# Kernel tuning notes

Hardware: AMD Instinct MI355X
Metric: run time of the kernel (lower is better)

## Reference

```python
import jax, jax.numpy as jnp
import numpy as np

N_NODES = 10000
N_EDGES = 640000
EMB_DIM = 128
NUM_LAYERS = 4
EPS_GIN = 0.0   # Tokenizer init eps
BN_EPS = 1e-5


def setup_inputs() -> dict:
    key = jax.random.key(0)
    k1, k2, k3 = jax.random.split(key, 3)
    x = jax.random.normal(k1, (N_NODES, EMB_DIM), dtype=jnp.float32)
    src = jax.random.randint(k2, (N_EDGES,), 0, N_NODES)
    dst = jax.random.randint(k3, (N_EDGES,), 0, N_NODES)
    gamma = jnp.ones((NUM_LAYERS, EMB_DIM), dtype=jnp.float32)
    beta = jnp.zeros((NUM_LAYERS, EMB_DIM), dtype=jnp.float32)
    return {"x": x, "gamma": gamma, "beta": beta, "src": src, "dst": dst}


def reference(x, gamma, beta, src, dst):
    # Tokenizer forward: num_layer x (NonParaGINConv -> BatchNorm1d), JK='last'
    n = x.shape[0]
    h = x
    for l in range(NUM_LAYERS):
        # GIN: neigh = sum over in-edges of source features (copy_u + fn.sum)
        neigh = jax.ops.segment_sum(h[src], dst, num_segments=n)
        h = (1.0 + EPS_GIN) * h + neigh
        # BatchNorm1d, training mode: biased batch statistics over nodes
        mu = jnp.mean(h, axis=0)
        var = jnp.var(h, axis=0)
        h = (h - mu) * jax.lax.rsqrt(var + BN_EPS) * gamma[l] + beta[l]
    return h  # JK == 'last'
```

## Files before the change

kernel.cpp:

```cpp
#include <hip/hip_runtime.h>

#define DIM 128
#define BN_EPS_F 1e-5f
#define NSLICE 16
#define MAXN 10240
#define CHUNKS 256

typedef unsigned int u32;
typedef unsigned short u16;

__device__ __forceinline__ float bflo(u32 w) {
    union { u32 u; float f; } c; c.u = w << 16; return c.f;
}
__device__ __forceinline__ float bfhi(u32 w) {
    union { u32 u; float f; } c; c.u = w & 0xffff0000u; return c.f;
}
__device__ __forceinline__ u32 packbf(float x, float y) {
    union { float f; u32 u; } ax, ay; ax.f = x; ay.f = y;
    u32 xr = (ax.u + 0x7fffu + ((ax.u >> 16) & 1u)) >> 16;
    u32 yr = (ay.u + 0x7fffu + ((ay.u >> 16) & 1u)) >> 16;
    return xr | (yr << 16);
}


__global__ __launch_bounds__(256) void chunkhist_kernel(const int* __restrict__ dst,
                                                        int* __restrict__ hist,
                                                        int n, int E, int chunk) {
    __shared__ int bins[MAXN];
    int tid = threadIdx.x;
    for (int i = tid; i < n; i += 256) bins[i] = 0;
    __syncthreads();
    int e0 = blockIdx.x * chunk;
    int e1 = min(e0 + chunk, E);
    for (int e = e0 + tid; e < e1; e += 256) atomicAdd(&bins[dst[e]], 1);
    __syncthreads();
    int* out = hist + (size_t)blockIdx.x * n;
    for (int i = tid; i < n; i += 256) out[i] = bins[i];
}

__global__ __launch_bounds__(256) void chunkscan_kernel(const int* __restrict__ hist,
                                                        int* __restrict__ chunkpref,
                                                        int* __restrict__ counts, int n) {
    int bin = blockIdx.x * 256 + threadIdx.x;
    if (bin >= n) return;
    const int* hp = hist + bin;
    int* cp = chunkpref + bin;
    int run = 0;
#pragma unroll 32
    for (int b = 0; b < CHUNKS; b++) {
        int v = hp[(size_t)b * n];
        cp[(size_t)b * n] = run;
        run += v;
    }
    counts[bin] = run;
}

__global__ __launch_bounds__(1024) void scan_kernel(const int* __restrict__ counts,
                                                    int* __restrict__ prowptr, int n) {
    __shared__ int sums[1024];
    const int CH = 16;
    int t = threadIdx.x;
    int base = t * CH;
    int local[CH];
    int s = 0;
#pragma unroll
    for (int i = 0; i < CH; i++) {
        int idx = base + i;
        local[i] = s;
        if (idx < n) s += (counts[idx] + 15) & ~15;
    }
    sums[t] = s;
    __syncthreads();
    for (int off = 1; off < 1024; off <<= 1) {
        int v = (t >= off) ? sums[t - off] : 0;
        __syncthreads();
        sums[t] += v;
        __syncthreads();
    }
    int prev = (t > 0) ? sums[t - 1] : 0;
#pragma unroll
    for (int i = 0; i < CH; i++) {
        int idx = base + i;
        if (idx < n) prowptr[idx] = prev + local[i];
    }
    if (t == 1023) prowptr[n] = sums[1023];
}

__global__ __launch_bounds__(256) void misc_kernel(const float* __restrict__ x,
                                                   u16* __restrict__ xb,
                                                   u16* __restrict__ r0,
                                                   u16* __restrict__ r1,
                                                   const int* __restrict__ prowptr,
                                                   const int* __restrict__ counts,
                                                   int* __restrict__ srcsorted,
                                                   float* __restrict__ gstats,
                                                   int total4, int n,
                                                   int nb_cvt, int nb_pad, int gtotal) {
    int bid = blockIdx.x;
    int tid = threadIdx.x;
    if (bid < nb_cvt) {
        int i = bid * 256 + tid;
        if (i < total4) {
            float4 v = ((const float4*)x)[i];
            uint2 w;
            w.x = packbf(v.x, v.y);
            w.y = packbf(v.z, v.w);
            *(uint2*)(xb + (size_t)i * 4) = w;
        } else {
            int j = i - total4;
            if (j < 96) {
                u16* t = (j < 32) ? xb : ((j < 64) ? r0 : r1);
                uint2 z; z.x = 0; z.y = 0;
                *(uint2*)(t + (size_t)n * DIM + (j & 31) * 4) = z;
            }
        }
    } else if (bid < nb_cvt + nb_pad) {
        int i = (bid - nb_cvt) * 256 + tid;
        if (i < n) {
            int pstart = prowptr[i];
            int c = counts[i];
            int p = (c + 15) & ~15;
            for (int k = c; k < p; k++) srcsorted[pstart + k] = n;
        }
    } else {
        int i = (bid - nb_cvt - nb_pad) * 256 + tid;
        if (i < gtotal) gstats[i] = 0.f;
    }
}

__global__ __launch_bounds__(256) void scatter_kernel(const int* __restrict__ src,
                                                      const int* __restrict__ dst,
                                                      const int* __restrict__ prowptr,
                                                      const int* __restrict__ chunkpref,
                                                      int* __restrict__ srcsorted,
                                                      int n, int E, int chunk) {
    __shared__ int cur[MAXN];
    int tid = threadIdx.x;
    const int* cp = chunkpref + (size_t)blockIdx.x * n;
    for (int i = tid; i < n; i += 256) cur[i] = prowptr[i] + cp[i];
    __syncthreads();
    int e0 = blockIdx.x * chunk;
    int e1 = min(e0 + chunk, E);
    for (int e = e0 + tid; e < e1; e += 256) {
        int d = dst[e];
        int pos = atomicAdd(&cur[d], 1);
        srcsorted[pos] = src[e];
    }
}

template <int USE_AB>
__global__ __launch_bounds__(256) void gather_kernel(
    const u16* __restrict__ hin, u16* __restrict__ hout,
    const int* __restrict__ prowptr, const int* __restrict__ counts,
    const int* __restrict__ srcs,
    const float* __restrict__ stats_in, float* __restrict__ stats_out,
    const float* __restrict__ gamma, const float* __restrict__ beta,
    int n, float inv_n) {
    __shared__ float ab_s[2 * DIM];
    __shared__ float part[2][DIM];
    __shared__ float ls[4][DIM];
    __shared__ float lq[4][DIM];
    int tid = threadIdx.x;
    int wid = tid >> 6;
    int node = blockIdx.x * 4 + wid;
    int lane = tid & 63;
    int grp = lane >> 4;
    int sub = lane & 15;

    if (USE_AB) {
        int c = tid & 127;
        int which = tid >> 7;
        const float* basep = stats_in + which * NSLICE * DIM + c;
        float acc = 0.f;
#pragma unroll
        for (int k = 0; k < NSLICE; k++) acc += basep[k * DIM];
        part[which][c] = acc;
        __syncthreads();
        if (tid < DIM) {
            float mu = part[0][tid] * inv_n;
            float var = part[1][tid] * inv_n - mu * mu;
            float av = gamma[tid] * rsqrtf(var + BN_EPS_F);
            ab_s[tid] = av;
            ab_s[DIM + tid] = beta[tid] - mu * av;
        }
        __syncthreads();
    }

    float r[8];
#pragma unroll
    for (int k = 0; k < 8; k++) r[k] = 0.f;

    if (node < n) {
        int start = prowptr[node];
        int pend = prowptr[node + 1];
        int deg = counts[node];
        const u16* hsub = hin + sub * 8;
        float acc[8];
#pragma unroll
        for (int k = 0; k < 8; k++) acc[k] = 0.f;

        int eb = start;
        for (; eb + 32 <= pend; eb += 32) {
            int e0 = eb + grp * 4;
            int s0 = srcs[e0 + 0];
            int s1 = srcs[e0 + 1];
            int s2 = srcs[e0 + 2];
            int s3 = srcs[e0 + 3];
            int s4 = srcs[e0 + 16];
            int s5 = srcs[e0 + 17];
            int s6 = srcs[e0 + 18];
            int s7 = srcs[e0 + 19];
            uint4 v0 = *(const uint4*)(hsub + (size_t)s0 * DIM);
            uint4 v1 = *(const uint4*)(hsub + (size_t)s1 * DIM);
            uint4 v2 = *(const uint4*)(hsub + (size_t)s2 * DIM);
            uint4 v3 = *(const uint4*)(hsub + (size_t)s3 * DIM);
            uint4 v4 = *(const uint4*)(hsub + (size_t)s4 * DIM);
            uint4 v5 = *(const uint4*)(hsub + (size_t)s5 * DIM);
            uint4 v6 = *(const uint4*)(hsub + (size_t)s6 * DIM);
            uint4 v7 = *(const uint4*)(hsub + (size_t)s7 * DIM);
            acc[0] += ((bflo(v0.x) + bflo(v1.x)) + (bflo(v2.x) + bflo(v3.x))) +
                      ((bflo(v4.x) + bflo(v5.x)) + (bflo(v6.x) + bflo(v7.x)));
            acc[1] += ((bfhi(v0.x) + bfhi(v1.x)) + (bfhi(v2.x) + bfhi(v3.x))) +
                      ((bfhi(v4.x) + bfhi(v5.x)) + (bfhi(v6.x) + bfhi(v7.x)));
            acc[2] += ((bflo(v0.y) + bflo(v1.y)) + (bflo(v2.y) + bflo(v3.y))) +
                      ((bflo(v4.y) + bflo(v5.y)) + (bflo(v6.y) + bflo(v7.y)));
            acc[3] += ((bfhi(v0.y) + bfhi(v1.y)) + (bfhi(v2.y) + bfhi(v3.y))) +
                      ((bfhi(v4.y) + bfhi(v5.y)) + (bfhi(v6.y) + bfhi(v7.y)));
            acc[4] += ((bflo(v0.z) + bflo(v1.z)) + (bflo(v2.z) + bflo(v3.z))) +
                      ((bflo(v4.z) + bflo(v5.z)) + (bflo(v6.z) + bflo(v7.z)));
            acc[5] += ((bfhi(v0.z) + bfhi(v1.z)) + (bfhi(v2.z) + bfhi(v3.z))) +
                      ((bfhi(v4.z) + bfhi(v5.z)) + (bfhi(v6.z) + bfhi(v7.z)));
            acc[6] += ((bflo(v0.w) + bflo(v1.w)) + (bflo(v2.w) + bflo(v3.w))) +
                      ((bflo(v4.w) + bflo(v5.w)) + (bflo(v6.w) + bflo(v7.w)));
            acc[7] += ((bfhi(v0.w) + bfhi(v1.w)) + (bfhi(v2.w) + bfhi(v3.w))) +
                      ((bfhi(v4.w) + bfhi(v5.w)) + (bfhi(v6.w) + bfhi(v7.w)));
        }
        if (eb < pend) {
            int e0 = eb + grp * 4;
            int s0 = srcs[e0 + 0];
            int s1 = srcs[e0 + 1];
            int s2 = srcs[e0 + 2];
            int s3 = srcs[e0 + 3];
            uint4 v0 = *(const uint4*)(hsub + (size_t)s0 * DIM);
            uint4 v1 = *(const uint4*)(hsub + (size_t)s1 * DIM);
            uint4 v2 = *(const uint4*)(hsub + (size_t)s2 * DIM);
            uint4 v3 = *(const uint4*)(hsub + (size_t)s3 * DIM);
            acc[0] += (bflo(v0.x) + bflo(v1.x)) + (bflo(v2.x) + bflo(v3.x));
            acc[1] += (bfhi(v0.x) + bfhi(v1.x)) + (bfhi(v2.x) + bfhi(v3.x));
            acc[2] += (bflo(v0.y) + bflo(v1.y)) + (bflo(v2.y) + bflo(v3.y));
            acc[3] += (bfhi(v0.y) + bfhi(v1.y)) + (bfhi(v2.y) + bfhi(v3.y));
            acc[4] += (bflo(v0.z) + bflo(v1.z)) + (bflo(v2.z) + bflo(v3.z));
            acc[5] += (bfhi(v0.z) + bfhi(v1.z)) + (bfhi(v2.z) + bfhi(v3.z));
            acc[6] += (bflo(v0.w) + bflo(v1.w)) + (bflo(v2.w) + bflo(v3.w));
            acc[7] += (bfhi(v0.w) + bfhi(v1.w)) + (bfhi(v2.w) + bfhi(v3.w));
        }
#pragma unroll
        for (int k = 0; k < 8; k++) {
            acc[k] += __shfl_xor(acc[k], 16);
            acc[k] += __shfl_xor(acc[k], 32);
        }

        uint4 sv = *(const uint4*)(hin + (size_t)node * DIM + sub * 8);
        float self[8] = {bflo(sv.x), bfhi(sv.x), bflo(sv.y), bfhi(sv.y),
                         bflo(sv.z), bfhi(sv.z), bflo(sv.w), bfhi(sv.w)};
        float degp1 = 1.0f + (float)deg;

        float av[8], bv[8];
        if (USE_AB) {
            float4 a0 = *(const float4*)(ab_s + sub * 8);
            float4 a1 = *(const float4*)(ab_s + sub * 8 + 4);
            float4 b0 = *(const float4*)(ab_s + DIM + sub * 8);
            float4 b1 = *(const float4*)(ab_s + DIM + sub * 8 + 4);
            av[0] = a0.x; av[1] = a0.y; av[2] = a0.z; av[3] = a0.w;
            av[4] = a1.x; av[5] = a1.y; av[6] = a1.z; av[7] = a1.w;
            bv[0] = b0.x; bv[1] = b0.y; bv[2] = b0.z; bv[3] = b0.w;
            bv[4] = b1.x; bv[5] = b1.y; bv[6] = b1.z; bv[7] = b1.w;
        } else {
#pragma unroll
            for (int k = 0; k < 8; k++) { av[k] = 1.f; bv[k] = 0.f; }
        }

        float o[8];
#pragma unroll
        for (int k = 0; k < 8; k++) o[k] = av[k] * (self[k] + acc[k]) + degp1 * bv[k];
        u32 w0 = packbf(o[0], o[1]);
        u32 w1 = packbf(o[2], o[3]);
        u32 w2 = packbf(o[4], o[5]);
        u32 w3 = packbf(o[6], o[7]);
        if (grp == 0) {
            uint4 wv; wv.x = w0; wv.y = w1; wv.z = w2; wv.w = w3;
            *(uint4*)(hout + (size_t)node * DIM + sub * 8) = wv;
        }
        r[0] = bflo(w0); r[1] = bfhi(w0); r[2] = bflo(w1); r[3] = bfhi(w1);
        r[4] = bflo(w2); r[5] = bfhi(w2); r[6] = bflo(w3); r[7] = bfhi(w3);
    }

    if (grp == 0) {
#pragma unroll
        for (int k = 0; k < 8; k++) {
            ls[wid][sub * 8 + k] = r[k];
            lq[wid][sub * 8 + k] = r[k] * r[k];
        }
    }
    __syncthreads();
    int slice = (blockIdx.x & (NSLICE - 1)) * DIM;
    int c = tid & 127;
    int which = tid >> 7;
    float s = which ? ((lq[0][c] + lq[1][c]) + (lq[2][c] + lq[3][c]))
                    : ((ls[0][c] + ls[1][c]) + (ls[2][c] + ls[3][c]));
    atomicAdd(&stats_out[which * NSLICE * DIM + slice + c], s);
}

__global__ __launch_bounds__(256) void apply_kernel(const u16* __restrict__ hb,
                                                    const float* __restrict__ stats_in,
                                                    const float* __restrict__ gamma,
                                                    const float* __restrict__ beta,
                                                    float* __restrict__ out, int total4,
                                                    float inv_n) {
    __shared__ float ab_s[2 * DIM];
    __shared__ float part[2][DIM];
    int tid = threadIdx.x;
    {
        int c = tid & 127;
        int which = tid >> 7;
        const float* basep = stats_in + which * NSLICE * DIM + c;
        float acc = 0.f;
#pragma unroll
        for (int k = 0; k < NSLICE; k++) acc += basep[k * DIM];
        part[which][c] = acc;
        __syncthreads();
        if (tid < DIM) {
            float mu = part[0][tid] * inv_n;
            float var = part[1][tid] * inv_n - mu * mu;
            float av = gamma[tid] * rsqrtf(var + BN_EPS_F);
            ab_s[tid] = av;
            ab_s[DIM + tid] = beta[tid] - mu * av;
        }
        __syncthreads();
    }
    for (int i = blockIdx.x * blockDim.x + tid; i < total4; i += gridDim.x * blockDim.x) {
        int quad = i & 31;
        uint2 w = *(const uint2*)(hb + (size_t)i * 4);
        const float4 a = *(const float4*)(ab_s + quad * 4);
        const float4 b = *(const float4*)(ab_s + DIM + quad * 4);
        float4 r;
        r.x = a.x * bflo(w.x) + b.x;
        r.y = a.y * bfhi(w.x) + b.y;
        r.z = a.z * bflo(w.y) + b.z;
        r.w = a.w * bfhi(w.y) + b.w;
        ((float4*)out)[i] = r;
    }
}

extern "C" void kernel_launch(void* const* d_in, const int* in_sizes, int n_in,
                              void* d_out, int out_size, void* d_ws, size_t ws_size,
                              hipStream_t stream) {
    const float* x = (const float*)d_in[0];
    const float* gamma = (const float*)d_in[1];
    const float* beta = (const float*)d_in[2];
    const int* src = (const int*)d_in[3];
    const int* dst = (const int*)d_in[4];
    float* out = (float*)d_out;

    const int n = in_sizes[0] / DIM;
    const int E = in_sizes[3];

    char* ws = (char*)d_ws;
    auto alloc = [&](size_t bytes) -> char* {
        char* p = ws;
        ws += (bytes + 255) / 256 * 256;
        return p;
    };
    const int STATS_PER_LAYER = 2 * NSLICE * DIM;
    int* prowptr = (int*)alloc((size_t)(n + 1) * 4);
    int* counts = (int*)alloc((size_t)n * 4);
    float* gstats = (float*)alloc((size_t)4 * STATS_PER_LAYER * 4);
    int* hist = (int*)alloc((size_t)CHUNKS * n * 4);
    int* chunkpref = (int*)alloc((size_t)CHUNKS * n * 4);
    int* srcsorted = (int*)alloc((size_t)(E + 16 * n) * 4);
    u16* hbx = (u16*)alloc((size_t)(n + 1) * DIM * 2);
    u16* hb0 = (u16*)alloc((size_t)(n + 1) * DIM * 2);
    u16* hb1 = (u16*)alloc((size_t)(n + 1) * DIM * 2);

    const int chunk = (E + CHUNKS - 1) / CHUNKS;
    const int total4 = n * DIM / 4;
    const int gtotal = 4 * STATS_PER_LAYER;
    const int NB_CVT = (total4 + 96 + 255) / 256;
    const int NB_PAD = (n + 255) / 256;
    const int NB_GZ = (gtotal + 255) / 256;

    chunkhist_kernel<<<CHUNKS, 256, 0, stream>>>(dst, hist, n, E, chunk);
    chunkscan_kernel<<<(n + 255) / 256, 256, 0, stream>>>(hist, chunkpref, counts, n);
    scan_kernel<<<1, 1024, 0, stream>>>(counts, prowptr, n);
    misc_kernel<<<NB_CVT + NB_PAD + NB_GZ, 256, 0, stream>>>(x, hbx, hb0, hb1, prowptr,
                                                             counts, srcsorted, gstats,
                                                             total4, n, NB_CVT, NB_PAD,
                                                             gtotal);
    scatter_kernel<<<CHUNKS, 256, 0, stream>>>(src, dst, prowptr, chunkpref, srcsorted,
                                               n, E, chunk);

    const int GB = (n + 3) / 4;
    const float inv_n = 1.0f / n;
    float* st0 = gstats + 0 * STATS_PER_LAYER;
    float* st1 = gstats + 1 * STATS_PER_LAYER;
    float* st2 = gstats + 2 * STATS_PER_LAYER;
    float* st3 = gstats + 3 * STATS_PER_LAYER;

    gather_kernel<0><<<GB, 256, 0, stream>>>(hbx, hb0, prowptr, counts, srcsorted,
                                             nullptr, st0, nullptr, nullptr, n, inv_n);
    gather_kernel<1><<<GB, 256, 0, stream>>>(hb0, hb1, prowptr, counts, srcsorted,
                                             st0, st1, gamma + 0 * DIM, beta + 0 * DIM,
                                             n, inv_n);
    gather_kernel<1><<<GB, 256, 0, stream>>>(hb1, hb0, prowptr, counts, srcsorted,
                                             st1, st2, gamma + 1 * DIM, beta + 1 * DIM,
                                             n, inv_n);
    gather_kernel<1><<<GB, 256, 0, stream>>>(hb0, hb1, prowptr, counts, srcsorted,
                                             st2, st3, gamma + 2 * DIM, beta + 2 * DIM,
                                             n, inv_n);
    apply_kernel<<<256, 256, 0, stream>>>(hb1, st3, gamma + 3 * DIM, beta + 3 * DIM, out,
                                          total4, inv_n);
}
```

Measured before the change: 180.2 us.

## Software-pipeline gather index loads and process two node groups per block

The gather kernel now prefetches the next batch of source indices while the current rows are being loaded and accumulated. Each block loops over two node groups and keeps BN partial sums in registers, which halves the grid and the number of stats atomics. The change also adds a launch-bounds occupancy hint and halves the histogram/scatter chunk count. The risks are fewer blocks to hide latency, higher register pressure from the prefetched indices, and a different float summation order.

```diff
diff --git a/kernel.cpp b/kernel.cpp
--- a/kernel.cpp
+++ b/kernel.cpp
@@ -4,7 +4,7 @@
 #define BN_EPS_F 1e-5f
 #define NSLICE 16
 #define MAXN 10240
-#define CHUNKS 256
+#define CHUNKS 128
 
 typedef unsigned int u32;
 typedef unsigned short u16;
@@ -20,6 +20,13 @@
     u32 xr = (ax.u + 0x7fffu + ((ax.u >> 16) & 1u)) >> 16;
     u32 yr = (ay.u + 0x7fffu + ((ay.u >> 16) & 1u)) >> 16;
     return xr | (yr << 16);
+}
+
+__device__ __forceinline__ void addrow(float* acc, const uint4 v) {
+    acc[0] += bflo(v.x); acc[1] += bfhi(v.x);
+    acc[2] += bflo(v.y); acc[3] += bfhi(v.y);
+    acc[4] += bflo(v.z); acc[5] += bfhi(v.z);
+    acc[6] += bflo(v.w); acc[7] += bfhi(v.w);
 }
 
 
@@ -149,20 +156,19 @@
 }
 
 template <int USE_AB>
-__global__ __launch_bounds__(256) void gather_kernel(
+__global__ __launch_bounds__(256, 4) void gather_kernel(
     const u16* __restrict__ hin, u16* __restrict__ hout,
     const int* __restrict__ prowptr, const int* __restrict__ counts,
     const int* __restrict__ srcs,
     const float* __restrict__ stats_in, float* __restrict__ stats_out,
     const float* __restrict__ gamma, const float* __restrict__ beta,
-    int n, float inv_n) {
+    int n, int ngroups, float inv_n) {
     __shared__ float ab_s[2 * DIM];
     __shared__ float part[2][DIM];
     __shared__ float ls[4][DIM];
     __shared__ float lq[4][DIM];
     int tid = threadIdx.x;
     int wid = tid >> 6;
-    int node = blockIdx.x * 4 + wid;
     int lane = tid & 63;
     int grp = lane >> 4;
     int sub = lane & 15;
@@ -186,11 +192,13 @@
         __syncthreads();
     }
 
-    float r[8];
-#pragma unroll
-    for (int k = 0; k < 8; k++) r[k] = 0.f;
-
-    if (node < n) {
+    float sacc[8], qacc[8];
+#pragma unroll
+    for (int k = 0; k < 8; k++) { sacc[k] = 0.f; qacc[k] = 0.f; }
+
+    for (int g = blockIdx.x; g < ngroups; g += gridDim.x) {
+        int node = g * 4 + wid;
+        if (node >= n) continue;
         int start = prowptr[node];
         int pend = prowptr[node + 1];
         int deg = counts[node];
@@ -200,59 +208,47 @@
         for (int k = 0; k < 8; k++) acc[k] = 0.f;
 
         int eb = start;
-        for (; eb + 32 <= pend; eb += 32) {
+        if (eb + 32 <= pend) {
             int e0 = eb + grp * 4;
-            int s0 = srcs[e0 + 0];
-            int s1 = srcs[e0 + 1];
-            int s2 = srcs[e0 + 2];
-            int s3 = srcs[e0 + 3];
-            int s4 = srcs[e0 + 16];
-            int s5 = srcs[e0 + 17];
-            int s6 = srcs[e0 + 18];
-            int s7 = srcs[e0 + 19];
+            int s0 = srcs[e0 + 0], s1 = srcs[e0 + 1];
+            int s2 = srcs[e0 + 2], s3 = srcs[e0 + 3];
+            int s4 = srcs[e0 + 16], s5 = srcs[e0 + 17];
+            int s6 = srcs[e0 + 18], s7 = srcs[e0 + 19];
+            while (true) {
+                uint4 v0 = *(const uint4*)(hsub + (size_t)s0 * DIM);
+                uint4 v1 = *(const uint4*)(hsub + (size_t)s1 * DIM);
+                uint4 v2 = *(const uint4*)(hsub + (size_t)s2 * DIM);
+                uint4 v3 = *(const uint4*)(hsub + (size_t)s3 * DIM);
+                uint4 v4 = *(const uint4*)(hsub + (size_t)s4 * DIM);
+                uint4 v5 = *(const uint4*)(hsub + (size_t)s5 * DIM);
+                uint4 v6 = *(const uint4*)(hsub + (size_t)s6 * DIM);
+                uint4 v7 = *(const uint4*)(hsub + (size_t)s7 * DIM);
+                int nb = eb + 32;
+                if (nb + 32 <= pend) {
+                    int e1 = nb + grp * 4;
+                    s0 = srcs[e1 + 0]; s1 = srcs[e1 + 1];
+                    s2 = srcs[e1 + 2]; s3 = srcs[e1 + 3];
+                    s4 = srcs[e1 + 16]; s5 = srcs[e1 + 17];
+                    s6 = srcs[e1 + 18]; s7 = srcs[e1 + 19];
+                }
+                addrow(acc, v0); addrow(acc, v1);
+                addrow(acc, v2); addrow(acc, v3);
+                addrow(acc, v4); addrow(acc, v5);
+                addrow(acc, v6); addrow(acc, v7);
+                eb = nb;
+                if (eb + 32 > pend) break;
+            }
+        }
+        if (eb < pend) {
+            int e0 = eb + grp * 4;
+            int s0 = srcs[e0 + 0], s1 = srcs[e0 + 1];
+            int s2 = srcs[e0 + 2], s3 = srcs[e0 + 3];
             uint4 v0 = *(const uint4*)(hsub + (size_t)s0 * DIM);
             uint4 v1 = *(const uint4*)(hsub + (size_t)s1 * DIM);
             uint4 v2 = *(const uint4*)(hsub + (size_t)s2 * DIM);
             uint4 v3 = *(const uint4*)(hsub + (size_t)s3 * DIM);
-            uint4 v4 = *(const uint4*)(hsub + (size_t)s4 * DIM);
-            uint4 v5 = *(const uint4*)(hsub + (size_t)s5 * DIM);
-            uint4 v6 = *(const uint4*)(hsub + (size_t)s6 * DIM);
-            uint4 v7 = *(const uint4*)(hsub + (size_t)s7 * DIM);
-            acc[0] += ((bflo(v0.x) + bflo(v1.x)) + (bflo(v2.x) + bflo(v3.x))) +
-                      ((bflo(v4.x) + bflo(v5.x)) + (bflo(v6.x) + bflo(v7.x)));
-            acc[1] += ((bfhi(v0.x) + bfhi(v1.x)) + (bfhi(v2.x) + bfhi(v3.x))) +
-                      ((bfhi(v4.x) + bfhi(v5.x)) + (bfhi(v6.x) + bfhi(v7.x)));
-            acc[2] += ((bflo(v0.y) + bflo(v1.y)) + (bflo(v2.y) + bflo(v3.y))) +
-                      ((bflo(v4.y) + bflo(v5.y)) + (bflo(v6.y) + bflo(v7.y)));
-            acc[3] += ((bfhi(v0.y) + bfhi(v1.y)) + (bfhi(v2.y) + bfhi(v3.y))) +
-                      ((bfhi(v4.y) + bfhi(v5.y)) + (bfhi(v6.y) + bfhi(v7.y)));
-            acc[4] += ((bflo(v0.z) + bflo(v1.z)) + (bflo(v2.z) + bflo(v3.z))) +
-                      ((bflo(v4.z) + bflo(v5.z)) + (bflo(v6.z) + bflo(v7.z)));
-            acc[5] += ((bfhi(v0.z) + bfhi(v1.z)) + (bfhi(v2.z) + bfhi(v3.z))) +
-                      ((bfhi(v4.z) + bfhi(v5.z)) + (bfhi(v6.z) + bfhi(v7.z)));
-            acc[6] += ((bflo(v0.w) + bflo(v1.w)) + (bflo(v2.w) + bflo(v3.w))) +
-                      ((bflo(v4.w) + bflo(v5.w)) + (bflo(v6.w) + bflo(v7.w)));
-            acc[7] += ((bfhi(v0.w) + bfhi(v1.w)) + (bfhi(v2.w) + bfhi(v3.w))) +
-                      ((bfhi(v4.w) + bfhi(v5.w)) + (bfhi(v6.w) + bfhi(v7.w)));
-        }
-        if (eb < pend) {
-            int e0 = eb + grp * 4;
-            int s0 = srcs[e0 + 0];
-            int s1 = srcs[e0 + 1];
-            int s2 = srcs[e0 + 2];
-            int s3 = srcs[e0 + 3];
-            uint4 v0 = *(const uint4*)(hsub + (size_t)s0 * DIM);
-            uint4 v1 = *(const uint4*)(hsub + (size_t)s1 * DIM);
-            uint4 v2 = *(const uint4*)(hsub + (size_t)s2 * DIM);
-            uint4 v3 = *(const uint4*)(hsub + (size_t)s3 * DIM);
-            acc[0] += (bflo(v0.x) + bflo(v1.x)) + (bflo(v2.x) + bflo(v3.x));
-            acc[1] += (bfhi(v0.x) + bfhi(v1.x)) + (bfhi(v2.x) + bfhi(v3.x));
-            acc[2] += (bflo(v0.y) + bflo(v1.y)) + (bflo(v2.y) + bflo(v3.y));
-            acc[3] += (bfhi(v0.y) + bfhi(v1.y)) + (bfhi(v2.y) + bfhi(v3.y));
-            acc[4] += (bflo(v0.z) + bflo(v1.z)) + (bflo(v2.z) + bflo(v3.z));
-            acc[5] += (bfhi(v0.z) + bfhi(v1.z)) + (bfhi(v2.z) + bfhi(v3.z));
-            acc[6] += (bflo(v0.w) + bflo(v1.w)) + (bflo(v2.w) + bflo(v3.w));
-            acc[7] += (bfhi(v0.w) + bfhi(v1.w)) + (bfhi(v2.w) + bfhi(v3.w));
+            addrow(acc, v0); addrow(acc, v1);
+            addrow(acc, v2); addrow(acc, v3);
         }
 #pragma unroll
         for (int k = 0; k < 8; k++) {
@@ -265,24 +261,24 @@
                          bflo(sv.z), bfhi(sv.z), bflo(sv.w), bfhi(sv.w)};
         float degp1 = 1.0f + (float)deg;
 
-        float av[8], bv[8];
+        float o[8];
         if (USE_AB) {
             float4 a0 = *(const float4*)(ab_s + sub * 8);
             float4 a1 = *(const float4*)(ab_s + sub * 8 + 4);
             float4 b0 = *(const float4*)(ab_s + DIM + sub * 8);
             float4 b1 = *(const float4*)(ab_s + DIM + sub * 8 + 4);
-            av[0] = a0.x; av[1] = a0.y; av[2] = a0.z; av[3] = a0.w;
-            av[4] = a1.x; av[5] = a1.y; av[6] = a1.z; av[7] = a1.w;
-            bv[0] = b0.x; bv[1] = b0.y; bv[2] = b0.z; bv[3] = b0.w;
-            bv[4] = b1.x; bv[5] = b1.y; bv[6] = b1.z; bv[7] = b1.w;
+            o[0] = a0.x * (self[0] + acc[0]) + degp1 * b0.x;
+            o[1] = a0.y * (self[1] + acc[1]) + degp1 * b0.y;
+            o[2] = a0.z * (self[2] + acc[2]) + degp1 * b0.z;
+            o[3] = a0.w * (self[3] + acc[3]) + degp1 * b0.w;
+            o[4] = a1.x * (self[4] + acc[4]) + degp1 * b1.x;
+            o[5] = a1.y * (self[5] + acc[5]) + degp1 * b1.y;
+            o[6] = a1.z * (self[6] + acc[6]) + degp1 * b1.z;
+            o[7] = a1.w * (self[7] + acc[7]) + degp1 * b1.w;
         } else {
 #pragma unroll
-            for (int k = 0; k < 8; k++) { av[k] = 1.f; bv[k] = 0.f; }
-        }
-
-        float o[8];
-#pragma unroll
-        for (int k = 0; k < 8; k++) o[k] = av[k] * (self[k] + acc[k]) + degp1 * bv[k];
+            for (int k = 0; k < 8; k++) o[k] = self[k] + acc[k];
+        }
         u32 w0 = packbf(o[0], o[1]);
         u32 w1 = packbf(o[2], o[3]);
         u32 w2 = packbf(o[4], o[5]);
@@ -291,15 +287,21 @@
             uint4 wv; wv.x = w0; wv.y = w1; wv.z = w2; wv.w = w3;
             *(uint4*)(hout + (size_t)node * DIM + sub * 8) = wv;
         }
-        r[0] = bflo(w0); r[1] = bfhi(w0); r[2] = bflo(w1); r[3] = bfhi(w1);
-        r[4] = bflo(w2); r[5] = bfhi(w2); r[6] = bflo(w3); r[7] = bfhi(w3);
-    }
-
+        float rr[8] = {bflo(w0), bfhi(w0), bflo(w1), bfhi(w1),
+                       bflo(w2), bfhi(w2), bflo(w3), bfhi(w3)};
+#pragma unroll
+        for (int k = 0; k < 8; k++) {
+            sacc[k] += rr[k];
+            qacc[k] += rr[k] * rr[k];
+        }
+    }
+
+    __syncthreads();
     if (grp == 0) {
 #pragma unroll
         for (int k = 0; k < 8; k++) {
-            ls[wid][sub * 8 + k] = r[k];
-            lq[wid][sub * 8 + k] = r[k] * r[k];
+            ls[wid][sub * 8 + k] = sacc[k];
+            lq[wid][sub * 8 + k] = qacc[k];
         }
     }
     __syncthreads();
@@ -399,7 +401,8 @@
     scatter_kernel<<<CHUNKS, 256, 0, stream>>>(src, dst, prowptr, chunkpref, srcsorted,
                                                n, E, chunk);
 
-    const int GB = (n + 3) / 4;
+    const int ngroups = (n + 3) / 4;
+    const int GB = (ngroups + 1) / 2;
     const float inv_n = 1.0f / n;
     float* st0 = gstats + 0 * STATS_PER_LAYER;
     float* st1 = gstats + 1 * STATS_PER_LAYER;
@@ -407,16 +410,17 @@
     float* st3 = gstats + 3 * STATS_PER_LAYER;
 
     gather_kernel<0><<<GB, 256, 0, stream>>>(hbx, hb0, prowptr, counts, srcsorted,
-                                             nullptr, st0, nullptr, nullptr, n, inv_n);
+                                             nullptr, st0, nullptr, nullptr, n, ngroups,
+                                             inv_n);
     gather_kernel<1><<<GB, 256, 0, stream>>>(hb0, hb1, prowptr, counts, srcsorted,
                                              st0, st1, gamma + 0 * DIM, beta + 0 * DIM,
-                                             n, inv_n);
+                                             n, ngroups, inv_n);
     gather_kernel<1><<<GB, 256, 0, stream>>>(hb1, hb0, prowptr, counts, srcsorted,
                                              st1, st2, gamma + 1 * DIM, beta + 1 * DIM,
-                                             n, inv_n);
+                                             n, ngroups, inv_n);
     gather_kernel<1><<<GB, 256, 0, stream>>>(hb0, hb1, prowptr, counts, srcsorted,
                                              st2, st3, gamma + 2 * DIM, beta + 2 * DIM,
-                                             n, inv_n);
+                                             n, ngroups, inv_n);
     apply_kernel<<<256, 256, 0, stream>>>(hb1, st3, gamma + 3 * DIM, beta + 3 * DIM, out,
                                           total4, inv_n);
 }
```

New measurement: 185.7 us. 1.03x slower.
